# Optimization experiments

Hardware: AMD Instinct MI355X
Metric: run time of the kernel (lower is better)

The kernel has to match this reference:

```python
import jax, jax.numpy as jnp
import numpy as np

N, E, G, T, H, ED, IN_D, OUT_D = 50000, 1600000, 64, 5, 64, 9, 10, 3
EPS = 1e-6

def _seg_mean(vals, seg, num):
    s = jax.ops.segment_sum(vals, seg, num_segments=num)
    c = jax.ops.segment_sum(jnp.ones((vals.shape[0],), vals.dtype), seg, num_segments=num)
    return s / jnp.maximum(c, 1.0)[:, None], c

def per_graph_edge_norm(edge_attr, edge_graph, num_graphs):
    # standardize each edge-feature column per graph (zero-shot transfer trick)
    mu, _ = _seg_mean(edge_attr, edge_graph, num_graphs)
    sq, _ = _seg_mean(edge_attr * edge_attr, edge_graph, num_graphs)
    var = jnp.maximum(sq - mu * mu, 0.0)
    std = jnp.sqrt(var)
    return (edge_attr - mu[edge_graph]) / (std[edge_graph] + EPS)

def setup_inputs() -> dict:
    key = jax.random.key(0)
    ks = jax.random.split(key, 24)
    s = 0.05  # weight scale to keep ReLU chains stable
    inp = {
        'x': jax.random.normal(ks[0], (N, IN_D), jnp.float32),
        'edge_index': jax.random.randint(ks[1], (2, E), 0, N),
        'edge_attr': jax.random.normal(ks[2], (E, ED), jnp.float32),
        'batch': jnp.sort(jax.random.randint(ks[3], (N,), 0, G)),
        'lift_W1': jax.random.normal(ks[4], (IN_D, H), jnp.float32) * s,
        'lift_b1': jnp.zeros((H,), jnp.float32),
        'lift_W2': jax.random.normal(ks[5], (H, H), jnp.float32) * s,
        'lift_b2': jnp.zeros((H,), jnp.float32),
        'Wself': jax.random.normal(ks[6], (T, H, H), jnp.float32) * s,
        'bself': jnp.zeros((T, H), jnp.float32),
        'msg_W0': jax.random.normal(ks[7], (T, H + ED, H), jnp.float32) * s,
        'msg_b0': jnp.zeros((T, H), jnp.float32),
        'msg_W1': jax.random.normal(ks[8], (T, H, H), jnp.float32) * s,
        'msg_b1': jnp.zeros((T, H), jnp.float32),
        'msg_W2': jax.random.normal(ks[9], (T, H, H), jnp.float32) * s,
        'msg_b2': jnp.zeros((T, H), jnp.float32),
        'gate_W': jax.random.normal(ks[10], (T, 1, H), jnp.float32) * s,
        'gate_b': jnp.zeros((T, H), jnp.float32),
        'proj_W1': jax.random.normal(ks[11], (H, H), jnp.float32) * s,
        'proj_b1': jnp.zeros((H,), jnp.float32),
        'proj_W2': jax.random.normal(ks[12], (H, OUT_D), jnp.float32) * s,
        'proj_b2': jnp.zeros((OUT_D,), jnp.float32),
    }
    return inp

def _gno(x, edge_index, edge_attr, batch,
         lift_W1, lift_b1, lift_W2, lift_b2,
         Wself, bself, msg_W0, msg_b0, msg_W1, msg_b1, msg_W2, msg_b2,
         gate_W, gate_b, proj_W1, proj_b1, proj_W2, proj_b2):
    src, dst = edge_index[0], edge_index[1]
    edge_graph = batch[src]
    ea = per_graph_edge_norm(edge_attr, edge_graph, G)  # cols 0:9 == all cols
    log_diag_y = x[:, 4:5]                               # [N,1]
    v0 = jax.nn.relu(x @ lift_W1 + lift_b1) @ lift_W2 + lift_b2  # lift
    v = v0
    for t in range(T):
        # gather -> per-edge MLP -> scatter-mean (AdmittanceKernelLayer)
        h = jnp.concatenate([v[src], ea], axis=-1)              # [E, H+ED]
        h = jax.nn.relu(h @ msg_W0[t] + msg_b0[t])
        h = jax.nn.relu(h @ msg_W1[t] + msg_b1[t])
        m = h @ msg_W2[t] + msg_b2[t]                           # [E, H]
        agg, _ = _seg_mean(m, dst, N)                           # mean aggregation
        gate = jax.nn.sigmoid(log_diag_y @ gate_W[t] + gate_b[t])  # [N,H]
        v = jax.nn.relu(v @ Wself[t] + bself[t] + agg + v0) * gate
        # dropout inactive at inference
    out = jax.nn.relu(v @ proj_W1 + proj_b1) @ proj_W2 + proj_b2  # project
    return out

def reference(x, edge_index, edge_attr, batch,
              lift_W1, lift_b1, lift_W2, lift_b2,
              Wself, bself, msg_W0, msg_b0, msg_W1, msg_b1, msg_W2, msg_b2,
              gate_W, gate_b, proj_W1, proj_b1, proj_W2, proj_b2):
    return _gno(x, edge_index, edge_attr, batch,
                lift_W1, lift_b1, lift_W2, lift_b2,
                Wself, bself, msg_W0, msg_b0, msg_W1, msg_b1, msg_W2, msg_b2,
                gate_W, gate_b, proj_W1, proj_b1, proj_W2, proj_b2)
```

## Files before the change

### kernel.cpp

```cpp
#include <hip/hip_runtime.h>
#include <math.h>

#define NN 50000
#define NE 1600000
#define NG 64
#define NT 5
#define NH 64
#define NED 9
#define NIN 10
#define NOUT 3
#define EPSF 1e-6f

typedef __attribute__((ext_vector_type(8))) short s8v;
typedef __attribute__((ext_vector_type(4))) short s4v;
typedef __attribute__((ext_vector_type(4))) float f32x4;

__device__ __forceinline__ unsigned short f2bf(float f) {
    union { float f; unsigned int u; } v; v.f = f;
    unsigned int r = v.u + 0x7FFFu + ((v.u >> 16) & 1u);
    return (unsigned short)(r >> 16);
}
__device__ __forceinline__ float bf2f(unsigned short b) {
    union { unsigned int u; float f; } v; v.u = ((unsigned int)b) << 16;
    return v.f;
}

__global__ void stats_kernel(const int* __restrict__ ei, const float* __restrict__ ea,
                             const int* __restrict__ batch,
                             float* __restrict__ ssum, float* __restrict__ ssq,
                             float* __restrict__ scnt) {
    __shared__ float lsum[NG * NED];
    __shared__ float lsq[NG * NED];
    __shared__ float lcnt[NG];
    for (int i = threadIdx.x; i < NG * NED; i += blockDim.x) { lsum[i] = 0.f; lsq[i] = 0.f; }
    for (int i = threadIdx.x; i < NG; i += blockDim.x) lcnt[i] = 0.f;
    __syncthreads();
    int lane = threadIdx.x & 63;
    int stride = gridDim.x * blockDim.x;
    for (int e = blockIdx.x * blockDim.x + threadIdx.x; e < NE; e += stride) {
        int s = ei[e];
        int g = batch[s];
        float a[NED];
#pragma unroll
        for (int d = 0; d < NED; ++d) a[d] = ea[(size_t)e * NED + d];
        int g0 = __builtin_amdgcn_readfirstlane(g);
        if (__all(g == g0)) {
            float sv[NED], qv[NED];
#pragma unroll
            for (int d = 0; d < NED; ++d) { sv[d] = a[d]; qv[d] = a[d] * a[d]; }
#pragma unroll
            for (int off = 32; off; off >>= 1) {
#pragma unroll
                for (int d = 0; d < NED; ++d) {
                    sv[d] += __shfl_down(sv[d], off);
                    qv[d] += __shfl_down(qv[d], off);
                }
            }
            if (lane == 0) {
#pragma unroll
                for (int d = 0; d < NED; ++d) {
                    atomicAdd(&lsum[g0 * NED + d], sv[d]);
                    atomicAdd(&lsq[g0 * NED + d], qv[d]);
                }
                atomicAdd(&lcnt[g0], 64.f);
            }
        } else {
            atomicAdd(&lcnt[g], 1.0f);
#pragma unroll
            for (int d = 0; d < NED; ++d) {
                atomicAdd(&lsum[g * NED + d], a[d]);
                atomicAdd(&lsq[g * NED + d], a[d] * a[d]);
            }
        }
    }
    __syncthreads();
    for (int i = threadIdx.x; i < NG * NED; i += blockDim.x) {
        atomicAdd(&ssum[i], lsum[i]);
        atomicAdd(&ssq[i], lsq[i]);
    }
    for (int i = threadIdx.x; i < NG; i += blockDim.x) atomicAdd(&scnt[i], lcnt[i]);
}

__global__ void stats_fin(const float* __restrict__ ssum, const float* __restrict__ ssq,
                          const float* __restrict__ scnt,
                          float* __restrict__ mu, float* __restrict__ rstd) {
    int i = blockIdx.x * blockDim.x + threadIdx.x;
    if (i >= NG * NED) return;
    int g = i / NED;
    float c = fmaxf(scnt[g], 1.0f);
    float m = ssum[i] / c;
    float q = ssq[i] / c;
    float var = fmaxf(q - m * m, 0.f);
    mu[i] = m;
    rstd[i] = 1.0f / (sqrtf(var) + EPSF);
}

__global__ void degint_kernel(const int* __restrict__ dst, int* __restrict__ ecnt) {
    int stride = gridDim.x * blockDim.x;
    for (int e = blockIdx.x * blockDim.x + threadIdx.x; e < NE; e += stride)
        atomicAdd(&ecnt[dst[e]], 1);
}

__global__ void scan1_kernel(const int* __restrict__ ecnt, int* __restrict__ partial) {
    __shared__ int sm[256];
    int i = blockIdx.x * 256 + threadIdx.x;
    sm[threadIdx.x] = (i < NN) ? ecnt[i] : 0;
    __syncthreads();
    for (int off = 128; off; off >>= 1) {
        if (threadIdx.x < off) sm[threadIdx.x] += sm[threadIdx.x + off];
        __syncthreads();
    }
    if (threadIdx.x == 0) partial[blockIdx.x] = sm[0];
}
__global__ void scan2_kernel(int* __restrict__ partial, int nb) {
    __shared__ int sm[256];
    int t = threadIdx.x;
    sm[t] = (t < nb) ? partial[t] : 0;
    __syncthreads();
    for (int off = 1; off < 256; off <<= 1) {
        int v = (t >= off) ? sm[t - off] : 0;
        __syncthreads();
        sm[t] += v;
        __syncthreads();
    }
    if (t < nb) partial[t] = (t ? sm[t - 1] : 0);
}
__global__ void scan3_kernel(const int* __restrict__ ecnt, const int* __restrict__ partial,
                             int* __restrict__ offs) {
    __shared__ int sm[256];
    int b = blockIdx.x, t = threadIdx.x, i = b * 256 + t;
    int x = (i < NN) ? ecnt[i] : 0;
    sm[t] = x;
    __syncthreads();
    for (int off = 1; off < 256; off <<= 1) {
        int v = (t >= off) ? sm[t - off] : 0;
        __syncthreads();
        sm[t] += v;
        __syncthreads();
    }
    if (i < NN) offs[i] = sm[t] - x + partial[b];
}

__global__ void permute_kernel(const int* __restrict__ ei, const int* __restrict__ offs,
                               int* __restrict__ cursor, int* __restrict__ perm) {
    int stride = gridDim.x * blockDim.x;
    for (int e = blockIdx.x * blockDim.x + threadIdx.x; e < NE; e += stride) {
        int d = ei[NE + e];
        int pos = offs[d] + atomicAdd(&cursor[d], 1);
        perm[pos] = e;
    }
}

__global__ void pack_kernel(const int* __restrict__ perm, const int* __restrict__ ei,
                            const float* __restrict__ ea, const int* __restrict__ batch,
                            const float* __restrict__ mu, const float* __restrict__ rstd,
                            int* __restrict__ srcPerm, int* __restrict__ dstPerm,
                            unsigned short* __restrict__ eaN) {
    int stride = gridDim.x * blockDim.x;
    for (int p = blockIdx.x * blockDim.x + threadIdx.x; p < NE; p += stride) {
        int e = perm[p];
        int s = ei[e], d = ei[NE + e];
        int g = batch[s];
        srcPerm[p] = s;
        dstPerm[p] = d;
#pragma unroll
        for (int k = 0; k < NED; ++k) {
            float val = (ea[(size_t)e * NED + k] - mu[g * NED + k]) * rstd[g * NED + k];
            eaN[(size_t)k * NE + p] = f2bf(val);
        }
    }
}

__global__ __launch_bounds__(256) void lift_kernel(
    const float* __restrict__ x,
    const float* __restrict__ W1, const float* __restrict__ b1,
    const float* __restrict__ W2, const float* __restrict__ b2,
    float* __restrict__ v0, float* __restrict__ v, float* __restrict__ ldy) {
    __shared__ float sW1[NIN * NH];
    __shared__ __align__(16) float sW2[NH][NH];
    __shared__ float sb1[NH], sb2[NH];
    for (int i = threadIdx.x; i < NIN * NH; i += blockDim.x) sW1[i] = W1[i];
    for (int i = threadIdx.x; i < NH * NH; i += blockDim.x) {
        int k = i >> 6, j = i & 63;
        sW2[j][k] = W2[i];
    }
    for (int i = threadIdx.x; i < NH; i += blockDim.x) { sb1[i] = b1[i]; sb2[i] = b2[i]; }
    __syncthreads();
    int stride = gridDim.x * blockDim.x;
    for (int n = blockIdx.x * blockDim.x + threadIdx.x; n < NN; n += stride) {
        float xr[NIN];
#pragma unroll
        for (int k = 0; k < NIN; ++k) xr[k] = x[(size_t)n * NIN + k];
        ldy[n] = xr[4];
        float h[NH];
#pragma unroll
        for (int j = 0; j < NH; ++j) {
            float acc = sb1[j];
#pragma unroll
            for (int k = 0; k < NIN; ++k) acc += xr[k] * sW1[k * NH + j];
            h[j] = fmaxf(acc, 0.f);
        }
#pragma unroll
        for (int j = 0; j < NH; ++j) {
            float acc = sb2[j];
#pragma unroll
            for (int k = 0; k < NH; k += 4) {
                float4 w = *(const float4*)&sW2[j][k];
                acc += h[k] * w.x + h[k + 1] * w.y + h[k + 2] * w.z + h[k + 3] * w.w;
            }
            v0[(size_t)n * NH + j] = acc;
            v[(size_t)n * NH + j] = acc;
        }
    }
}

__device__ __forceinline__ void gemm_acc68(const float* __restrict__ Ab,
                                           const float* __restrict__ Wb,
                                           int K, int te, int tj, float acc[4][4]) {
#pragma unroll 4
    for (int k = 0; k < K; ++k) {
        float4 a = *(const float4*)(Ab + k * 68 + (te << 2));
        float4 b = *(const float4*)(Wb + (k << 6) + (tj << 2));
        acc[0][0] = fmaf(a.x, b.x, acc[0][0]);
        acc[0][1] = fmaf(a.x, b.y, acc[0][1]);
        acc[0][2] = fmaf(a.x, b.z, acc[0][2]);
        acc[0][3] = fmaf(a.x, b.w, acc[0][3]);
        acc[1][0] = fmaf(a.y, b.x, acc[1][0]);
        acc[1][1] = fmaf(a.y, b.y, acc[1][1]);
        acc[1][2] = fmaf(a.y, b.z, acc[1][2]);
        acc[1][3] = fmaf(a.y, b.w, acc[1][3]);
        acc[2][0] = fmaf(a.z, b.x, acc[2][0]);
        acc[2][1] = fmaf(a.z, b.y, acc[2][1]);
        acc[2][2] = fmaf(a.z, b.z, acc[2][2]);
        acc[2][3] = fmaf(a.z, b.w, acc[2][3]);
        acc[3][0] = fmaf(a.w, b.x, acc[3][0]);
        acc[3][1] = fmaf(a.w, b.y, acc[3][1]);
        acc[3][2] = fmaf(a.w, b.z, acc[3][2]);
        acc[3][3] = fmaf(a.w, b.w, acc[3][3]);
    }
}

__global__ __launch_bounds__(256, 4) void u_kernel(
    const float* __restrict__ v, const float* __restrict__ W0v,
    const float* __restrict__ b0, float* __restrict__ U) {
    __shared__ __align__(16) float Vt[64][68];
    __shared__ __align__(16) float sW[64][64];
    __shared__ float sb[64];
    const int tid = threadIdx.x;
    const int base = blockIdx.x * 64;
    const int te = tid >> 4, tj = tid & 15;

    {
        int r = tid >> 2;
        int kb = (tid & 3) << 4;
        int n = base + r;
        const float4* vrow = (const float4*)(v + (size_t)n * NH + kb);
#pragma unroll
        for (int q = 0; q < 4; ++q) {
            float4 f = (n < NN) ? vrow[q] : make_float4(0.f, 0.f, 0.f, 0.f);
            int k = kb + q * 4;
            Vt[k + 0][r] = f.x; Vt[k + 1][r] = f.y; Vt[k + 2][r] = f.z; Vt[k + 3][r] = f.w;
        }
    }
    for (int i4 = tid; i4 < 64 * 16; i4 += 256) {
        int k = i4 >> 4, c4 = i4 & 15;
        *(float4*)&sW[k][c4 * 4] = *(const float4*)(W0v + (size_t)k * 64 + c4 * 4);
    }
    if (tid < 64) sb[tid] = b0[tid];
    __syncthreads();

    float acc[4][4];
    {
        float b0_ = sb[tj * 4 + 0], b1_ = sb[tj * 4 + 1], b2_ = sb[tj * 4 + 2], b3_ = sb[tj * 4 + 3];
#pragma unroll
        for (int ee = 0; ee < 4; ++ee) { acc[ee][0] = b0_; acc[ee][1] = b1_; acc[ee][2] = b2_; acc[ee][3] = b3_; }
    }
    gemm_acc68(&Vt[0][0], &sW[0][0], 64, te, tj, acc);

#pragma unroll
    for (int ee = 0; ee < 4; ++ee) {
        int n = base + te * 4 + ee;
        if (n < NN)
            *(float4*)&U[(size_t)n * NH + tj * 4] =
                make_float4(acc[ee][0], acc[ee][1], acc[ee][2], acc[ee][3]);
    }
}

__global__ __launch_bounds__(256, 4) void edge3_kernel(
    const int* __restrict__ srcPerm, const int* __restrict__ dstPerm,
    const unsigned short* __restrict__ eaN,
    const float* __restrict__ W0e, const float* __restrict__ W1, const float* __restrict__ b1,
    const float* __restrict__ U, float* __restrict__ nodesum) {
    __shared__ __align__(16) float Ubuf[64][68];
    __shared__ __align__(16) float sEa[NED][68];
    __shared__ __align__(16) float sWe[NED][64];
    __shared__ __align__(16) short h0bf[64 * 64];
    __shared__ __align__(16) short W1bf[64 * 64];
    __shared__ float sb1[64];
    __shared__ int sDst[64];

    const int tid = threadIdx.x;
    const int base = blockIdx.x * 64;
    const int te = tid >> 4, tj = tid & 15;

    if (tid < 64) { sDst[tid] = dstPerm[base + tid]; sb1[tid] = b1[tid]; }
    {
        int r = tid >> 2;
        int kb = (tid & 3) << 4;
        int s = srcPerm[base + r];
        const float4* urow = (const float4*)(U + (size_t)s * NH + kb);
#pragma unroll
        for (int q = 0; q < 4; ++q)
            *(float4*)&Ubuf[r][kb + q * 4] = urow[q];
    }
    for (int i = tid; i < NED * 64; i += 256) {
        int d = i >> 6, c = i & 63;
        sEa[d][c] = bf2f(eaN[(size_t)d * NE + base + c]);
    }
    for (int i4 = tid; i4 < NED * 16; i4 += 256) {
        int k = i4 >> 4, c4 = i4 & 15;
        *(float4*)&sWe[k][c4 * 4] = *(const float4*)(W0e + (size_t)k * 64 + c4 * 4);
    }
    for (int i4 = tid; i4 < 64 * 16; i4 += 256) {
        int k = i4 >> 4, j4 = (i4 & 15) * 4;
        float4 wv = *(const float4*)(W1 + (size_t)k * 64 + j4);
        unsigned short wb[4] = { f2bf(wv.x), f2bf(wv.y), f2bf(wv.z), f2bf(wv.w) };
        int kb = k * 2;
#pragma unroll
        for (int jj = 0; jj < 4; ++jj) {
            int row = j4 + jj;
            *(short*)((char*)W1bf + row * 128 + (kb ^ ((row & 7) << 4))) = (short)wb[jj];
        }
    }
    __syncthreads();

    float acc0[4][4];
#pragma unroll
    for (int ee = 0; ee < 4; ++ee) {
        float4 u4 = *(const float4*)&Ubuf[te * 4 + ee][tj * 4];
        acc0[ee][0] = u4.x; acc0[ee][1] = u4.y; acc0[ee][2] = u4.z; acc0[ee][3] = u4.w;
    }
    gemm_acc68(&sEa[0][0], &sWe[0][0], NED, te, tj, acc0);

#pragma unroll
    for (int ee = 0; ee < 4; ++ee) {
        int row = te * 4 + ee;
        s4v p;
        p[0] = (short)f2bf(fmaxf(acc0[ee][0], 0.f));
        p[1] = (short)f2bf(fmaxf(acc0[ee][1], 0.f));
        p[2] = (short)f2bf(fmaxf(acc0[ee][2], 0.f));
        p[3] = (short)f2bf(fmaxf(acc0[ee][3], 0.f));
        *(s4v*)((char*)h0bf + row * 128 + ((tj * 8) ^ ((row & 7) << 4))) = p;
    }
    __syncthreads();

    const int lane = tid & 63, w = tid >> 6;
    const int l15 = lane & 15, l4 = lane >> 4;
    f32x4 acc[4];
#pragma unroll
    for (int c = 0; c < 4; ++c) {
        float b = sb1[16 * c + l15];
        acc[c][0] = b; acc[c][1] = b; acc[c][2] = b; acc[c][3] = b;
    }
    {
        const int arow = 16 * w + l15;
        const char* abase = (const char*)h0bf + arow * 128;
        const int aswz = (arow & 7) << 4;
#pragma unroll
        for (int kc = 0; kc < 2; ++kc) {
            s8v af = *(const s8v*)(abase + ((16 * l4 + 64 * kc) ^ aswz));
#pragma unroll
            for (int c = 0; c < 4; ++c) {
                int brow = 16 * c + l15;
                s8v bf = *(const s8v*)((const char*)W1bf + brow * 128 +
                                       ((16 * l4 + 64 * kc) ^ ((brow & 7) << 4)));
                acc[c] = __builtin_amdgcn_mfma_f32_16x16x32_bf16(af, bf, acc[c], 0, 0, 0);
            }
        }
    }

#pragma unroll
    for (int r = 0; r < 4; ++r) {
        int erow = 16 * w + 4 * l4 + r;
#pragma unroll
        for (int c = 0; c < 4; ++c)
            Ubuf[erow][16 * c + l15] = fmaxf(acc[c][r], 0.f);
    }
    __syncthreads();

    {
        int c = tid & 63;
        int r0 = 16 * w;
        int cur = sDst[r0];
        float a = Ubuf[r0][c];
#pragma unroll
        for (int i = 1; i < 16; ++i) {
            int d = sDst[r0 + i];
            float hv = Ubuf[r0 + i][c];
            if (d != cur) {
                atomicAdd(&nodesum[(size_t)cur * NH + c], a);
                cur = d;
                a = hv;
            } else {
                a += hv;
            }
        }
        atomicAdd(&nodesum[(size_t)cur * NH + c], a);
    }
}

__global__ __launch_bounds__(256, 2) void update3_kernel(
    const float* __restrict__ Wself, const float* __restrict__ bself,
    const float* __restrict__ W2, const float* __restrict__ b2,
    const float* __restrict__ gWt, const float* __restrict__ gbt,
    const float* __restrict__ v0, const float* __restrict__ ldy,
    const int* __restrict__ ecnt, const float* __restrict__ nodesum,
    float* __restrict__ v) {
    __shared__ __align__(16) float Vt[64][68];
    __shared__ __align__(16) float St[64][68];
    __shared__ __align__(16) float sWs[64][64];
    __shared__ __align__(16) float sW2[64][64];
    __shared__ float sbs[64], sb2[64], sgw[64], sgb[64];
    const int tid = threadIdx.x;
    const int base = blockIdx.x * 64;
    const int te = tid >> 4, tj = tid & 15;

    {
        int r = tid >> 2;
        int kb = (tid & 3) << 4;
        int n = base + r;
        const float4* vrow = (const float4*)(v + (size_t)n * NH + kb);
        const float4* srow = (const float4*)(nodesum + (size_t)n * NH + kb);
#pragma unroll
        for (int q = 0; q < 4; ++q) {
            float4 f = (n < NN) ? vrow[q] : make_float4(0.f, 0.f, 0.f, 0.f);
            float4 g = (n < NN) ? srow[q] : make_float4(0.f, 0.f, 0.f, 0.f);
            int k = kb + q * 4;
            Vt[k + 0][r] = f.x; Vt[k + 1][r] = f.y; Vt[k + 2][r] = f.z; Vt[k + 3][r] = f.w;
            St[k + 0][r] = g.x; St[k + 1][r] = g.y; St[k + 2][r] = g.z; St[k + 3][r] = g.w;
        }
    }
    for (int i4 = tid; i4 < 64 * 16; i4 += 256) {
        int k = i4 >> 4, c4 = i4 & 15;
        *(float4*)&sWs[k][c4 * 4] = *(const float4*)(Wself + (size_t)k * 64 + c4 * 4);
        *(float4*)&sW2[k][c4 * 4] = *(const float4*)(W2 + (size_t)k * 64 + c4 * 4);
    }
    if (tid < 64) { sbs[tid] = bself[tid]; sb2[tid] = b2[tid]; sgw[tid] = gWt[tid]; sgb[tid] = gbt[tid]; }
    __syncthreads();

    float acc1[4][4], acc2[4][4];
    {
        float b0_ = sbs[tj * 4 + 0], b1_ = sbs[tj * 4 + 1], b2_ = sbs[tj * 4 + 2], b3_ = sbs[tj * 4 + 3];
#pragma unroll
        for (int ee = 0; ee < 4; ++ee) {
            acc1[ee][0] = b0_; acc1[ee][1] = b1_; acc1[ee][2] = b2_; acc1[ee][3] = b3_;
            acc2[ee][0] = 0.f; acc2[ee][1] = 0.f; acc2[ee][2] = 0.f; acc2[ee][3] = 0.f;
        }
    }
    gemm_acc68(&Vt[0][0], &sWs[0][0], 64, te, tj, acc1);
    gemm_acc68(&St[0][0], &sW2[0][0], 64, te, tj, acc2);

    float gw0 = sgw[tj * 4 + 0], gw1 = sgw[tj * 4 + 1], gw2 = sgw[tj * 4 + 2], gw3 = sgw[tj * 4 + 3];
    float gb0 = sgb[tj * 4 + 0], gb1 = sgb[tj * 4 + 1], gb2 = sgb[tj * 4 + 2], gb3 = sgb[tj * 4 + 3];
    float bb0 = sb2[tj * 4 + 0], bb1 = sb2[tj * 4 + 1], bb2 = sb2[tj * 4 + 2], bb3 = sb2[tj * 4 + 3];
#pragma unroll
    for (int ee = 0; ee < 4; ++ee) {
        int n = base + te * 4 + ee;
        if (n >= NN) continue;
        float cnt = (float)ecnt[n];
        float has = (cnt > 0.5f) ? 1.f : 0.f;
        float dninv = has / fmaxf(cnt, 1.f);
        float ld = ldy[n];
        float4 v0r = *(const float4*)&v0[(size_t)n * NH + tj * 4];
        float z0 = acc1[ee][0] + acc2[ee][0] * dninv + bb0 * has + v0r.x;
        float z1 = acc1[ee][1] + acc2[ee][1] * dninv + bb1 * has + v0r.y;
        float z2 = acc1[ee][2] + acc2[ee][2] * dninv + bb2 * has + v0r.z;
        float z3 = acc1[ee][3] + acc2[ee][3] * dninv + bb3 * has + v0r.w;
        float g0 = 1.f / (1.f + expf(-(ld * gw0 + gb0)));
        float g1 = 1.f / (1.f + expf(-(ld * gw1 + gb1)));
        float g2 = 1.f / (1.f + expf(-(ld * gw2 + gb2)));
        float g3 = 1.f / (1.f + expf(-(ld * gw3 + gb3)));
        *(float4*)&v[(size_t)n * NH + tj * 4] =
            make_float4(fmaxf(z0, 0.f) * g0, fmaxf(z1, 0.f) * g1,
                        fmaxf(z2, 0.f) * g2, fmaxf(z3, 0.f) * g3);
    }
}

__global__ __launch_bounds__(256) void proj_kernel(
    const float* __restrict__ v,
    const float* __restrict__ pW1, const float* __restrict__ pb1,
    const float* __restrict__ pW2, const float* __restrict__ pb2,
    float* __restrict__ out) {
    __shared__ __align__(16) float sW1[NH][NH];
    __shared__ float sb1[NH];
    __shared__ float sW2[NH * NOUT];
    __shared__ float sb2[NOUT];
    for (int i = threadIdx.x; i < NH * NH; i += blockDim.x) {
        int k = i >> 6, j = i & 63;
        sW1[j][k] = pW1[i];
    }
    for (int i = threadIdx.x; i < NH; i += blockDim.x) sb1[i] = pb1[i];
    for (int i = threadIdx.x; i < NH * NOUT; i += blockDim.x) sW2[i] = pW2[i];
    for (int i = threadIdx.x; i < NOUT; i += blockDim.x) sb2[i] = pb2[i];
    __syncthreads();
    int stride = gridDim.x * blockDim.x;
    for (int n = blockIdx.x * blockDim.x + threadIdx.x; n < NN; n += stride) {
        float vr[NH];
        const float4* vp = (const float4*)(v + (size_t)n * NH);
#pragma unroll
        for (int q = 0; q < NH / 4; ++q) {
            float4 f = vp[q];
            vr[4 * q + 0] = f.x; vr[4 * q + 1] = f.y; vr[4 * q + 2] = f.z; vr[4 * q + 3] = f.w;
        }
        float o0 = sb2[0], o1 = sb2[1], o2 = sb2[2];
#pragma unroll
        for (int j = 0; j < NH; ++j) {
            float acc = sb1[j];
#pragma unroll
            for (int k = 0; k < NH; k += 4) {
                float4 w = *(const float4*)&sW1[j][k];
                acc += vr[k] * w.x + vr[k + 1] * w.y + vr[k + 2] * w.z + vr[k + 3] * w.w;
            }
            float h = fmaxf(acc, 0.f);
            o0 += h * sW2[j * NOUT + 0];
            o1 += h * sW2[j * NOUT + 1];
            o2 += h * sW2[j * NOUT + 2];
        }
        out[(size_t)n * NOUT + 0] = o0;
        out[(size_t)n * NOUT + 1] = o1;
        out[(size_t)n * NOUT + 2] = o2;
    }
}

extern "C" void kernel_launch(void* const* d_in, const int* in_sizes, int n_in,
                              void* d_out, int out_size, void* d_ws, size_t ws_size,
                              hipStream_t stream) {
    (void)in_sizes; (void)n_in; (void)out_size; (void)ws_size;
    const float* x     = (const float*)d_in[0];
    const int*   ei    = (const int*)d_in[1];
    const float* ea    = (const float*)d_in[2];
    const int*   batch = (const int*)d_in[3];
    const float* lW1   = (const float*)d_in[4];
    const float* lb1   = (const float*)d_in[5];
    const float* lW2   = (const float*)d_in[6];
    const float* lb2   = (const float*)d_in[7];
    const float* Wself = (const float*)d_in[8];
    const float* bself = (const float*)d_in[9];
    const float* mW0   = (const float*)d_in[10];
    const float* mb0   = (const float*)d_in[11];
    const float* mW1   = (const float*)d_in[12];
    const float* mb1   = (const float*)d_in[13];
    const float* mW2   = (const float*)d_in[14];
    const float* mb2   = (const float*)d_in[15];
    const float* gW    = (const float*)d_in[16];
    const float* gb    = (const float*)d_in[17];
    const float* pW1   = (const float*)d_in[18];
    const float* pb1   = (const float*)d_in[19];
    const float* pW2   = (const float*)d_in[20];
    const float* pb2   = (const float*)d_in[21];
    float* out = (float*)d_out;
    float* ws  = (float*)d_ws;

    float* nodesum = ws;
    float* v0   = nodesum + (size_t)NN * NH;
    float* v    = v0 + (size_t)NN * NH;
    float* U    = v + (size_t)NN * NH;
    float* ldy  = U + (size_t)NN * NH;
    float* mu   = ldy + NN;
    float* rstd = mu + NG * NED;
    float* ssum = rstd + NG * NED;
    float* ssq  = ssum + NG * NED;
    float* scnt = ssq + NG * NED;
    int*   ecnt   = (int*)(scnt + NG);
    int*   cursor = ecnt + NN;
    int*   offs    = cursor + NN;
    int*   partial = offs + NN;
    int*   srcPerm = partial + 256;
    int*   dstPerm = srcPerm + NE;
    unsigned short* eaN = (unsigned short*)(dstPerm + NE);
    int*   perm = (int*)nodesum;

    const int NBLK = (NN + 63) / 64;
    const int SBLK = (NN + 255) / 256;

    hipMemsetAsync(ssum, 0, ((size_t)(2 * NG * NED + NG) + 2 * NN) * sizeof(float), stream);

    stats_kernel<<<512, 256, 0, stream>>>(ei, ea, batch, ssum, ssq, scnt);
    stats_fin<<<3, 256, 0, stream>>>(ssum, ssq, scnt, mu, rstd);
    degint_kernel<<<2048, 256, 0, stream>>>(ei + NE, ecnt);
    scan1_kernel<<<SBLK, 256, 0, stream>>>(ecnt, partial);
    scan2_kernel<<<1, 256, 0, stream>>>(partial, SBLK);
    scan3_kernel<<<SBLK, 256, 0, stream>>>(ecnt, partial, offs);
    permute_kernel<<<2048, 256, 0, stream>>>(ei, offs, cursor, perm);
    pack_kernel<<<2048, 256, 0, stream>>>(perm, ei, ea, batch, mu, rstd, srcPerm, dstPerm, eaN);
    lift_kernel<<<200, 256, 0, stream>>>(x, lW1, lb1, lW2, lb2, v0, v, ldy);

    for (int t = 0; t < NT; ++t) {
        const float* W0t = mW0 + (size_t)t * (NH + NED) * NH;
        hipMemsetAsync(nodesum, 0, (size_t)NN * NH * sizeof(float), stream);
        u_kernel<<<NBLK, 256, 0, stream>>>(v, W0t, mb0 + (size_t)t * NH, U);
        edge3_kernel<<<NE / 64, 256, 0, stream>>>(
            srcPerm, dstPerm, eaN,
            W0t + (size_t)NH * NH,
            mW1 + (size_t)t * NH * NH, mb1 + (size_t)t * NH,
            U, nodesum);
        update3_kernel<<<NBLK, 256, 0, stream>>>(
            Wself + (size_t)t * NH * NH, bself + (size_t)t * NH,
            mW2 + (size_t)t * NH * NH, mb2 + (size_t)t * NH,
            gW + (size_t)t * NH, gb + (size_t)t * NH,
            v0, ldy, ecnt, nodesum, v);
    }
    proj_kernel<<<200, 256, 0, stream>>>(v, pW1, pb1, pW2, pb2, out);
}
```

Baseline: 1.611 ms.

## Make edge kernel persistent per-wave with fragment-packed weights and segment-uniform fast path

The edge MLP kernel becomes persistent: 1024 blocks whose waves each loop over 16-edge subtiles. The W1 MFMA fragments and W0e are staged once per block instead of once per 64-edge block, and per-wave buffers remove block-wide barriers. U rows and edge features are loaded straight into registers. When all 16 edges share one destination, a shuffle reduction issues a single atomic per column. The in-degree count is also folded into the stats kernel, which drops one launch and one pass over dst, at the cost of extra atomics in the stats loop.

```diff
diff --git a/kernel.cpp b/kernel.cpp
--- a/kernel.cpp
+++ b/kernel.cpp
@@ -10,6 +10,7 @@
 #define NIN 10
 #define NOUT 3
 #define EPSF 1e-6f
+#define NSUB (NE / 16)
 
 typedef __attribute__((ext_vector_type(8))) short s8v;
 typedef __attribute__((ext_vector_type(4))) short s4v;
@@ -28,7 +29,7 @@
 __global__ void stats_kernel(const int* __restrict__ ei, const float* __restrict__ ea,
                              const int* __restrict__ batch,
                              float* __restrict__ ssum, float* __restrict__ ssq,
-                             float* __restrict__ scnt) {
+                             float* __restrict__ scnt, int* __restrict__ ecnt) {
     __shared__ float lsum[NG * NED];
     __shared__ float lsq[NG * NED];
     __shared__ float lcnt[NG];
@@ -40,6 +41,7 @@
     for (int e = blockIdx.x * blockDim.x + threadIdx.x; e < NE; e += stride) {
         int s = ei[e];
         int g = batch[s];
+        atomicAdd(&ecnt[ei[NE + e]], 1);
         float a[NED];
 #pragma unroll
         for (int d = 0; d < NED; ++d) a[d] = ea[(size_t)e * NED + d];
@@ -93,12 +95,6 @@
     float var = fmaxf(q - m * m, 0.f);
     mu[i] = m;
     rstd[i] = 1.0f / (sqrtf(var) + EPSF);
-}
-
-__global__ void degint_kernel(const int* __restrict__ dst, int* __restrict__ ecnt) {
-    int stride = gridDim.x * blockDim.x;
-    for (int e = blockIdx.x * blockDim.x + threadIdx.x; e < NE; e += stride)
-        atomicAdd(&ecnt[dst[e]], 1);
 }
 
 __global__ void scan1_kernel(const int* __restrict__ ecnt, int* __restrict__ partial) {
@@ -286,126 +282,148 @@
     }
 }
 
-__global__ __launch_bounds__(256, 4) void edge3_kernel(
+__global__ __launch_bounds__(256, 4) void edge4_kernel(
     const int* __restrict__ srcPerm, const int* __restrict__ dstPerm,
     const unsigned short* __restrict__ eaN,
     const float* __restrict__ W0e, const float* __restrict__ W1, const float* __restrict__ b1,
     const float* __restrict__ U, float* __restrict__ nodesum) {
-    __shared__ __align__(16) float Ubuf[64][68];
-    __shared__ __align__(16) float sEa[NED][68];
     __shared__ __align__(16) float sWe[NED][64];
-    __shared__ __align__(16) short h0bf[64 * 64];
-    __shared__ __align__(16) short W1bf[64 * 64];
-    __shared__ float sb1[64];
-    __shared__ int sDst[64];
+    __shared__ __align__(16) short W1frag[8][64][8];
+    __shared__ __align__(16) short h0bf[4][16 * 64];
+    __shared__ __align__(16) float h1s[4][16 * 64];
+    __shared__ int sDstS[4][16];
 
     const int tid = threadIdx.x;
-    const int base = blockIdx.x * 64;
-    const int te = tid >> 4, tj = tid & 15;
-
-    if (tid < 64) { sDst[tid] = dstPerm[base + tid]; sb1[tid] = b1[tid]; }
-    {
-        int r = tid >> 2;
-        int kb = (tid & 3) << 4;
-        int s = srcPerm[base + r];
-        const float4* urow = (const float4*)(U + (size_t)s * NH + kb);
-#pragma unroll
-        for (int q = 0; q < 4; ++q)
-            *(float4*)&Ubuf[r][kb + q * 4] = urow[q];
-    }
-    for (int i = tid; i < NED * 64; i += 256) {
-        int d = i >> 6, c = i & 63;
-        sEa[d][c] = bf2f(eaN[(size_t)d * NE + base + c]);
-    }
+    const int lane = tid & 63, w = tid >> 6;
+    const int l15 = lane & 15, l4 = lane >> 4;
+
     for (int i4 = tid; i4 < NED * 16; i4 += 256) {
         int k = i4 >> 4, c4 = i4 & 15;
         *(float4*)&sWe[k][c4 * 4] = *(const float4*)(W0e + (size_t)k * 64 + c4 * 4);
     }
-    for (int i4 = tid; i4 < 64 * 16; i4 += 256) {
-        int k = i4 >> 4, j4 = (i4 & 15) * 4;
-        float4 wv = *(const float4*)(W1 + (size_t)k * 64 + j4);
-        unsigned short wb[4] = { f2bf(wv.x), f2bf(wv.y), f2bf(wv.z), f2bf(wv.w) };
-        int kb = k * 2;
-#pragma unroll
-        for (int jj = 0; jj < 4; ++jj) {
-            int row = j4 + jj;
-            *(short*)((char*)W1bf + row * 128 + (kb ^ ((row & 7) << 4))) = (short)wb[jj];
-        }
-    }
-    __syncthreads();
-
-    float acc0[4][4];
-#pragma unroll
-    for (int ee = 0; ee < 4; ++ee) {
-        float4 u4 = *(const float4*)&Ubuf[te * 4 + ee][tj * 4];
-        acc0[ee][0] = u4.x; acc0[ee][1] = u4.y; acc0[ee][2] = u4.z; acc0[ee][3] = u4.w;
-    }
-    gemm_acc68(&sEa[0][0], &sWe[0][0], NED, te, tj, acc0);
-
-#pragma unroll
-    for (int ee = 0; ee < 4; ++ee) {
-        int row = te * 4 + ee;
-        s4v p;
-        p[0] = (short)f2bf(fmaxf(acc0[ee][0], 0.f));
-        p[1] = (short)f2bf(fmaxf(acc0[ee][1], 0.f));
-        p[2] = (short)f2bf(fmaxf(acc0[ee][2], 0.f));
-        p[3] = (short)f2bf(fmaxf(acc0[ee][3], 0.f));
-        *(s4v*)((char*)h0bf + row * 128 + ((tj * 8) ^ ((row & 7) << 4))) = p;
-    }
-    __syncthreads();
-
-    const int lane = tid & 63, w = tid >> 6;
-    const int l15 = lane & 15, l4 = lane >> 4;
-    f32x4 acc[4];
-#pragma unroll
-    for (int c = 0; c < 4; ++c) {
-        float b = sb1[16 * c + l15];
-        acc[c][0] = b; acc[c][1] = b; acc[c][2] = b; acc[c][3] = b;
-    }
-    {
-        const int arow = 16 * w + l15;
-        const char* abase = (const char*)h0bf + arow * 128;
-        const int aswz = (arow & 7) << 4;
-#pragma unroll
-        for (int kc = 0; kc < 2; ++kc) {
-            s8v af = *(const s8v*)(abase + ((16 * l4 + 64 * kc) ^ aswz));
+    for (int idx = tid; idx < 2 * 4 * 64; idx += 256) {
+        int kc = idx >> 8, c = (idx >> 6) & 3, ln = idx & 63;
+        int fl15 = ln & 15, fl4 = ln >> 4;
+        int col = 16 * c + fl15;
+        s8v frag;
+#pragma unroll
+        for (int j = 0; j < 8; ++j) {
+            int k = kc * 32 + fl4 * 8 + j;
+            frag[j] = (short)f2bf(W1[(size_t)k * 64 + col]);
+        }
+        *(s8v*)&W1frag[kc * 4 + c][ln][0] = frag;
+    }
+    float b1r[4];
+#pragma unroll
+    for (int c = 0; c < 4; ++c) b1r[c] = b1[16 * c + l15];
+    __syncthreads();
+
+    short* myh0 = h0bf[w];
+    float* myh1 = h1s[w];
+    int*   myd  = sDstS[w];
+    const int gw = blockIdx.x * 4 + w;
+    const int nw = gridDim.x * 4;
+
+    for (int st = gw; st < NSUB; st += nw) {
+        const int e16 = st * 16;
+        if (lane < 16) myd[lane] = dstPerm[e16 + lane];
+
+        int4 s4 = *(const int4*)(srcPerm + e16 + 4 * l4);
+        ushort4 eu[NED];
+#pragma unroll
+        for (int d = 0; d < NED; ++d)
+            eu[d] = *(const ushort4*)(eaN + (size_t)d * NE + e16 + 4 * l4);
+
+        float acc0[4][4];
+        {
+            const int* sp = (const int*)&s4;
+#pragma unroll
+            for (int ee = 0; ee < 4; ++ee) {
+                float4 u4 = *(const float4*)(U + (size_t)sp[ee] * NH + 4 * l15);
+                acc0[ee][0] = u4.x; acc0[ee][1] = u4.y; acc0[ee][2] = u4.z; acc0[ee][3] = u4.w;
+            }
+        }
+#pragma unroll
+        for (int d = 0; d < NED; ++d) {
+            float4 wv = *(const float4*)&sWe[d][4 * l15];
+            float a0 = bf2f(eu[d].x), a1 = bf2f(eu[d].y), a2 = bf2f(eu[d].z), a3 = bf2f(eu[d].w);
+            acc0[0][0] = fmaf(a0, wv.x, acc0[0][0]); acc0[0][1] = fmaf(a0, wv.y, acc0[0][1]);
+            acc0[0][2] = fmaf(a0, wv.z, acc0[0][2]); acc0[0][3] = fmaf(a0, wv.w, acc0[0][3]);
+            acc0[1][0] = fmaf(a1, wv.x, acc0[1][0]); acc0[1][1] = fmaf(a1, wv.y, acc0[1][1]);
+            acc0[1][2] = fmaf(a1, wv.z, acc0[1][2]); acc0[1][3] = fmaf(a1, wv.w, acc0[1][3]);
+            acc0[2][0] = fmaf(a2, wv.x, acc0[2][0]); acc0[2][1] = fmaf(a2, wv.y, acc0[2][1]);
+            acc0[2][2] = fmaf(a2, wv.z, acc0[2][2]); acc0[2][3] = fmaf(a2, wv.w, acc0[2][3]);
+            acc0[3][0] = fmaf(a3, wv.x, acc0[3][0]); acc0[3][1] = fmaf(a3, wv.y, acc0[3][1]);
+            acc0[3][2] = fmaf(a3, wv.z, acc0[3][2]); acc0[3][3] = fmaf(a3, wv.w, acc0[3][3]);
+        }
+
+#pragma unroll
+        for (int ee = 0; ee < 4; ++ee) {
+            int row = 4 * l4 + ee;
+            s4v p;
+            p[0] = (short)f2bf(fmaxf(acc0[ee][0], 0.f));
+            p[1] = (short)f2bf(fmaxf(acc0[ee][1], 0.f));
+            p[2] = (short)f2bf(fmaxf(acc0[ee][2], 0.f));
+            p[3] = (short)f2bf(fmaxf(acc0[ee][3], 0.f));
+            *(s4v*)((char*)myh0 + row * 128 + ((l15 * 8) ^ ((row & 7) << 4))) = p;
+        }
+
+        f32x4 acc[4];
+#pragma unroll
+        for (int c = 0; c < 4; ++c) {
+            float b = b1r[c];
+            acc[c][0] = b; acc[c][1] = b; acc[c][2] = b; acc[c][3] = b;
+        }
+        {
+            const char* abase = (const char*)myh0 + l15 * 128;
+            const int aswz = (l15 & 7) << 4;
+#pragma unroll
+            for (int kc = 0; kc < 2; ++kc) {
+                s8v af = *(const s8v*)(abase + ((l4 * 16 + kc * 64) ^ aswz));
+#pragma unroll
+                for (int c = 0; c < 4; ++c) {
+                    s8v bf = *(const s8v*)&W1frag[kc * 4 + c][lane][0];
+                    acc[c] = __builtin_amdgcn_mfma_f32_16x16x32_bf16(af, bf, acc[c], 0, 0, 0);
+                }
+            }
+        }
+
+        int dFirst = myd[0];
+        int dLast = myd[15];
+        if (dFirst == dLast) {
 #pragma unroll
             for (int c = 0; c < 4; ++c) {
-                int brow = 16 * c + l15;
-                s8v bf = *(const s8v*)((const char*)W1bf + brow * 128 +
-                                       ((16 * l4 + 64 * kc) ^ ((brow & 7) << 4)));
-                acc[c] = __builtin_amdgcn_mfma_f32_16x16x32_bf16(af, bf, acc[c], 0, 0, 0);
-            }
-        }
-    }
-
-#pragma unroll
-    for (int r = 0; r < 4; ++r) {
-        int erow = 16 * w + 4 * l4 + r;
-#pragma unroll
-        for (int c = 0; c < 4; ++c)
-            Ubuf[erow][16 * c + l15] = fmaxf(acc[c][r], 0.f);
-    }
-    __syncthreads();
-
-    {
-        int c = tid & 63;
-        int r0 = 16 * w;
-        int cur = sDst[r0];
-        float a = Ubuf[r0][c];
-#pragma unroll
-        for (int i = 1; i < 16; ++i) {
-            int d = sDst[r0 + i];
-            float hv = Ubuf[r0 + i][c];
-            if (d != cur) {
-                atomicAdd(&nodesum[(size_t)cur * NH + c], a);
-                cur = d;
-                a = hv;
-            } else {
-                a += hv;
-            }
-        }
-        atomicAdd(&nodesum[(size_t)cur * NH + c], a);
+                float vs = fmaxf(acc[c][0], 0.f) + fmaxf(acc[c][1], 0.f) +
+                           fmaxf(acc[c][2], 0.f) + fmaxf(acc[c][3], 0.f);
+                vs += __shfl_xor(vs, 16);
+                vs += __shfl_xor(vs, 32);
+                if (l4 == 0)
+                    atomicAdd(&nodesum[(size_t)dFirst * NH + 16 * c + l15], vs);
+            }
+        } else {
+#pragma unroll
+            for (int r = 0; r < 4; ++r) {
+                int row = 4 * l4 + r;
+#pragma unroll
+                for (int c = 0; c < 4; ++c)
+                    myh1[row * 64 + ((16 * c + l15) ^ (l4 * 8))] = fmaxf(acc[c][r], 0.f);
+            }
+            int cur = dFirst;
+            float a = myh1[lane];
+#pragma unroll
+            for (int i = 1; i < 16; ++i) {
+                int dn = myd[i];
+                float hv = myh1[i * 64 + (lane ^ ((i >> 2) * 8))];
+                if (dn != cur) {
+                    atomicAdd(&nodesum[(size_t)cur * NH + lane], a);
+                    cur = dn;
+                    a = hv;
+                } else {
+                    a += hv;
+                }
+            }
+            atomicAdd(&nodesum[(size_t)cur * NH + lane], a);
+        }
     }
 }
 
@@ -585,9 +603,8 @@
 
     hipMemsetAsync(ssum, 0, ((size_t)(2 * NG * NED + NG) + 2 * NN) * sizeof(float), stream);
 
-    stats_kernel<<<512, 256, 0, stream>>>(ei, ea, batch, ssum, ssq, scnt);
+    stats_kernel<<<512, 256, 0, stream>>>(ei, ea, batch, ssum, ssq, scnt, ecnt);
     stats_fin<<<3, 256, 0, stream>>>(ssum, ssq, scnt, mu, rstd);
-    degint_kernel<<<2048, 256, 0, stream>>>(ei + NE, ecnt);
     scan1_kernel<<<SBLK, 256, 0, stream>>>(ecnt, partial);
     scan2_kernel<<<1, 256, 0, stream>>>(partial, SBLK);
     scan3_kernel<<<SBLK, 256, 0, stream>>>(ecnt, partial, offs);
@@ -599,7 +616,7 @@
         const float* W0t = mW0 + (size_t)t * (NH + NED) * NH;
         hipMemsetAsync(nodesum, 0, (size_t)NN * NH * sizeof(float), stream);
         u_kernel<<<NBLK, 256, 0, stream>>>(v, W0t, mb0 + (size_t)t * NH, U);
-        edge3_kernel<<<NE / 64, 256, 0, stream>>>(
+        edge4_kernel<<<1024, 256, 0, stream>>>(
             srcPerm, dstPerm, eaN,
             W0t + (size_t)NH * NH,
             mW1 + (size_t)t * NH * NH, mb1 + (size_t)t * NH,
```

New measurement: 1.366 ms. -15.2%, faster.
